# Performance work log

Measured on AMD Instinct MI355X. Metric: run time of the kernel, lower is better.

The kernel has to match this reference:

```python
import jax, jax.numpy as jnp
import numpy as np

ROUTINGS = 3

def squash(s, axis=-1):
    # drives long vectors toward length 1, short vectors toward 0
    norm = jnp.linalg.norm(s, axis=axis, keepdims=True)
    scale = norm ** 2 / (1.0 + norm ** 2) / (norm + 1e-8)
    return scale * s

def dense_capsule(x, W, routings=ROUTINGS):
    # x: [B, I, Di], W: [O, I, Do, Di] -> out: [B, O, Do]
    # torch.matmul(W, x[:,None,:,:,None]).squeeze(-1) == einsum over Di
    x_hat = jnp.einsum('oidc,bic->boid', W, x)          # [B, O, I, Do]
    x_hat_det = jax.lax.stop_gradient(x_hat)
    B, O, I, _ = x_hat.shape
    b = jnp.zeros((B, O, I), dtype=x_hat.dtype)
    outputs = None
    for i in range(routings):
        c = jax.nn.softmax(b, axis=1)                    # [B, O, I]
        if i == routings - 1:
            outputs = squash(jnp.sum(c[..., None] * x_hat, axis=2, keepdims=True))
        else:
            outputs = squash(jnp.sum(c[..., None] * x_hat_det, axis=2, keepdims=True))
            b = b + jnp.sum(outputs * x_hat_det, axis=-1)
    return jnp.squeeze(outputs, axis=2)                  # [B, O, Do]

INIT_NUM_CAP = 128
INIT_DIM_CAP = 8

def setup_inputs() -> dict:
    key = jax.random.key(0)
    k0, k1, k2, k3 = jax.random.split(key, 4)
    x = jax.random.normal(k0, (1024, 1024), dtype=jnp.float32)
    W0 = 0.01 * jax.random.normal(k1, (64, 128, 16, 8), dtype=jnp.float32)
    W1 = 0.01 * jax.random.normal(k2, (32, 64, 32, 16), dtype=jnp.float32)
    W2 = 0.01 * jax.random.normal(k3, (10, 32, 64, 32), dtype=jnp.float32)
    return {"x": x, "W0": W0, "W1": W1, "W2": W2}

def reference(x, W0, W1, W2):
    h = x.reshape(-1, INIT_NUM_CAP, INIT_DIM_CAP)        # [B, 128, 8]
    for W in (W0, W1, W2):
        h = dense_capsule(h, W)
    return jnp.linalg.norm(h, axis=-1)                   # [B, 10]
```

## Files before the change

kernel.cpp:

```cpp
#include <hip/hip_runtime.h>
#include <math.h>

typedef unsigned int u32;

__device__ __forceinline__ u32 pk2(float a, float b){
    u32 ua=__float_as_uint(a), ub=__float_as_uint(b);
    u32 ra=(ua + 0x7fffu + ((ua>>16)&1u))>>16;
    u32 rb=(ub + 0x7fffu + ((ub>>16)&1u))>>16;
    return ra | (rb<<16);
}
__device__ __forceinline__ float lo16(u32 p){ return __uint_as_float(p<<16); }
__device__ __forceinline__ float hi16(u32 p){ return __uint_as_float(p & 0xffff0000u); }

#if __has_builtin(__builtin_amdgcn_fdot2_f32_bf16)
__device__ __forceinline__ float dot2bf(u32 a, u32 b, float c){
    float d;
    asm("v_dot2_f32_bf16 %0, %1, %2, %3" : "=v"(d) : "v"(a), "v"(b), "v"(c));
    return d;
}
#else
__device__ __forceinline__ float dot2bf(u32 a, u32 b, float c){
    return fmaf(hi16(a), hi16(b), fmaf(lo16(a), lo16(b), c));
}
#endif

__device__ __forceinline__ void gll16(const u32* gp, u32* lp){
    __builtin_amdgcn_global_load_lds((const __attribute__((address_space(1))) void*)gp,
                                     (__attribute__((address_space(3))) void*)lp,
                                     16, 0, 0);
}

template<int I,int Di,int O,int Do,int IR>
__global__ void k_conv(const float* __restrict__ W, u32* __restrict__ Wb){
    constexpr int CB=Di/8, LPO=Do/16, GR=LPO*O, NSL=16*CB;
    const int n = O*I*Do*Di/2;
    for (int t = blockIdx.x*blockDim.x+threadIdx.x; t < n; t += gridDim.x*blockDim.x){
        int cw = t & 3;
        int u4 = t >> 2;
        int g    = u4 % GR;  int r1 = u4 / GR;
        int slot = r1 % NSL; int r2 = r1 / NSL;
        int il   = r2 % IR;  int si = r2 / IR;
        int i  = si*IR + il;
        int j  = slot / CB, cb = slot % CB;
        int o  = g % O,     q  = g / O;
        int jg = q*16 + j;
        int c  = cb*8 + cw*2;
        const float* src = W + ((size_t)(o*I + i)*Do + jg)*Di + c;
        Wb[t] = pk2(src[0], src[1]);
    }
}

__global__ void k_pack(const float* __restrict__ x, u32* __restrict__ hb){
    int t = blockIdx.x*blockDim.x + threadIdx.x;
    if (t < 1024*512){
        float2 f = ((const float2*)x)[t];
        hb[t] = pk2(f.x, f.y);
    }
}

template<int I,int Di,int O,int Do,int IR,bool LOGIT>
__global__ __launch_bounds__(512,2) void k_contract(
    const u32* __restrict__ Wb, const u32* __restrict__ hsrc,
    const u32* __restrict__ vsb, u32* __restrict__ ps)
{
    constexpr int CB=Di/8, LPO=Do/16, ACT=O*LPO, GR=LPO*O, NSL=16*CB;
    constexpr int SLICE  = IR*NSL*GR*4;
    constexpr int ROUNDS = SLICE/2048;
    static_assert(SLICE <= 16384, "64KB slab");
    static_assert(SLICE % 2048 == 0, "staging granularity");
    __shared__ __align__(16) u32 slab[SLICE];

    const int tid = threadIdx.x;
    const int w = tid>>6, l = tid&63;
    const int eg = blockIdx.x, sp = blockIdx.y;

    const bool act = l < ACT;
    const int qL = act ? (l%LPO) : 0;
    const int oL = act ? (l/LPO) : 0;
    const int lnoff = qL*O + oL;
    const uint4* W4 = (const uint4*)slab;

    const int e0 = eg*16 + w*2;

    u32 vp[2][8];
    if constexpr (LOGIT){
        #pragma unroll
        for (int k=0;k<2;++k){
            uint4 a = *(const uint4*)(vsb + (size_t)(e0+k)*512 + l*8);
            uint4 b = *(const uint4*)(vsb + (size_t)(e0+k)*512 + l*8 + 4);
            vp[k][0]=a.x; vp[k][1]=a.y; vp[k][2]=a.z; vp[k][3]=a.w;
            vp[k][4]=b.x; vp[k][5]=b.y; vp[k][6]=b.z; vp[k][7]=b.w;
        }
    }

    float sacc[2][16];
    #pragma unroll
    for (int k=0;k<2;++k)
        #pragma unroll
        for (int j=0;j<16;++j) sacc[k][j]=0.f;

    for (int sub=0; sub<2; ++sub){
        if (sub) __syncthreads();
        {
            const u32* g = Wb + (size_t)(sp*2+sub)*SLICE + tid*4;
            u32* ld = slab + w*256;
            #pragma unroll
            for (int rd=0; rd<ROUNDS; ++rd) gll16(g + rd*2048, ld + rd*2048);
        }
        __syncthreads();

        #pragma unroll
        for (int il=0; il<IR; ++il){
            const int i = (sp*2+sub)*IR + il;

            float xh[2][16];
            #pragma unroll
            for (int k=0;k<2;++k)
                #pragma unroll
                for (int j=0;j<16;++j) xh[k][j]=0.f;

            #pragma unroll
            for (int cb=0; cb<CB; ++cb){
                u32 hk[2][4];
                #pragma unroll
                for (int k=0;k<2;++k){
                    uint4 hv = *(const uint4*)(hsrc + (size_t)(e0+k)*512 + i*(Di/2) + cb*4);
                    hk[k][0]=hv.x; hk[k][1]=hv.y; hk[k][2]=hv.z; hk[k][3]=hv.w;
                }
                #pragma unroll
                for (int j=0;j<16;++j){
                    uint4 wv = W4[(il*NSL + j*CB + cb)*GR + lnoff];
                    #pragma unroll
                    for (int k=0;k<2;++k){
                        float t = xh[k][j];
                        t = dot2bf(wv.x, hk[k][0], t);
                        t = dot2bf(wv.y, hk[k][1], t);
                        t = dot2bf(wv.z, hk[k][2], t);
                        t = dot2bf(wv.w, hk[k][3], t);
                        xh[k][j] = t;
                    }
                }
            }

            float cc[2];
            if constexpr (!LOGIT){
                cc[0]=1.f; cc[1]=1.f;
            } else {
                #pragma unroll
                for (int k=0;k<2;++k){
                    float lp=0.f;
                    #pragma unroll
                    for (int jj=0;jj<8;++jj)
                        lp += lo16(vp[k][jj])*xh[k][2*jj] + hi16(vp[k][jj])*xh[k][2*jj+1];
                    if constexpr (LPO>=2) lp += __shfl_xor(lp,1,64);
                    if constexpr (LPO>=4) lp += __shfl_xor(lp,2,64);
                    float ev = act ? __expf(lp) : 0.f;
                    float tot = ev;
                    tot+=__shfl_xor(tot,1,64);  tot+=__shfl_xor(tot,2,64);
                    tot+=__shfl_xor(tot,4,64);  tot+=__shfl_xor(tot,8,64);
                    tot+=__shfl_xor(tot,16,64); tot+=__shfl_xor(tot,32,64);
                    cc[k] = ev*(float)LPO/tot;
                }
            }
            #pragma unroll
            for (int k=0;k<2;++k)
                #pragma unroll
                for (int j=0;j<16;++j) sacc[k][j] += cc[k]*xh[k][j];
        }
    }

    if (act){
        #pragma unroll
        for (int k=0;k<2;++k){
            u32* pp = ps + ((size_t)(sp*1024 + e0 + k))*512 + l*8;
            uint4 o0, o1;
            o0.x=pk2(sacc[k][0],sacc[k][1]);   o0.y=pk2(sacc[k][2],sacc[k][3]);
            o0.z=pk2(sacc[k][4],sacc[k][5]);   o0.w=pk2(sacc[k][6],sacc[k][7]);
            o1.x=pk2(sacc[k][8],sacc[k][9]);   o1.y=pk2(sacc[k][10],sacc[k][11]);
            o1.z=pk2(sacc[k][12],sacc[k][13]); o1.w=pk2(sacc[k][14],sacc[k][15]);
            *(uint4*)pp = o0;
            *(uint4*)(pp+4) = o1;
        }
    }
}

template<int O,int Do,int MODE>
__global__ __launch_bounds__(256) void k_squash(
    const u32* __restrict__ ps, u32* __restrict__ vsb, void* __restrict__ dst)
{
    constexpr int LPO=Do/16, ACT=O*LPO;
    const int tid=threadIdx.x, w=tid>>6, l=tid&63;
    const int e = blockIdx.x*4 + w;
    const bool act = l < ACT;
    const int oL = act ? (l/LPO) : 0;

    float s[16];
    #pragma unroll
    for (int j=0;j<16;++j) s[j]=0.f;
    #pragma unroll
    for (int si=0; si<16; ++si){
        const u32* pp = ps + ((size_t)(si*1024 + e))*512 + l*8;
        uint4 a = *(const uint4*)pp;
        uint4 b = *(const uint4*)(pp+4);
        u32 q[8] = {a.x,a.y,a.z,a.w,b.x,b.y,b.z,b.w};
        #pragma unroll
        for (int k=0;k<8;++k){ s[2*k] += lo16(q[k]); s[2*k+1] += hi16(q[k]); }
    }
    if constexpr (MODE==0){
        #pragma unroll
        for (int j=0;j<16;++j) s[j] *= (1.0f/(float)O);
    }
    float n2=0.f;
    #pragma unroll
    for (int j=0;j<16;++j) n2 += s[j]*s[j];
    if constexpr (LPO>=2) n2 += __shfl_xor(n2,1,64);
    if constexpr (LPO>=4) n2 += __shfl_xor(n2,2,64);
    float nrm   = sqrtf(n2);
    float scale = n2/((1.f+n2)*(nrm+1e-8f));

    if constexpr (MODE==0){
        if (act){
            u32* vp = vsb + (size_t)e*512 + l*8;
            #pragma unroll
            for (int k=0;k<8;++k) vp[k] = pk2(scale*s[2*k], scale*s[2*k+1]);
        }
    } else if constexpr (MODE==1){
        if (act){
            u32* vp = vsb + (size_t)e*512 + l*8;
            #pragma unroll
            for (int k=0;k<8;++k){
                u32 old = vp[k];
                vp[k] = pk2(lo16(old)+scale*s[2*k], hi16(old)+scale*s[2*k+1]);
            }
        }
    } else if constexpr (MODE==2){
        if (act){
            u32* hp = (u32*)dst + (size_t)e*512 + l*8;
            #pragma unroll
            for (int k=0;k<8;++k) hp[k] = pk2(scale*s[2*k], scale*s[2*k+1]);
        }
    } else {
        float q=0.f;
        #pragma unroll
        for (int j=0;j<16;++j){ float vj=scale*s[j]; q += vj*vj; }
        if constexpr (LPO>=2) q += __shfl_xor(q,1,64);
        if constexpr (LPO>=4) q += __shfl_xor(q,2,64);
        if (act && (l%LPO)==0)
            ((float*)dst)[(size_t)e*O + oL] = sqrtf(q);
    }
}

template<int I, int Di, int O, int Do, bool FINAL>
__device__ __forceinline__ void fb_layer(const float* __restrict__ W, float* __restrict__ hl,
                                         float* __restrict__ out, int e, int l) {
    constexpr int LPO = Do / 16;
    constexpr int ACT = O * LPO;
    const int o  = l / LPO;
    const int d0 = (l % LPO) * 16;
    const bool act = (l < ACT);
    float vs[16];
    #pragma unroll
    for (int j = 0; j < 16; ++j) vs[j] = 0.f;
    for (int r = 0; r < 3; ++r) {
        float sacc[16];
        #pragma unroll
        for (int j = 0; j < 16; ++j) sacc[j] = 0.f;
        for (int i = 0; i < I; ++i) {
            if ((i & 15) == 0) __syncthreads();
            float xh[16];
            #pragma unroll
            for (int j = 0; j < 16; ++j) xh[j] = 0.f;
            if (act) {
                const float* wb = W + ((size_t)(o * I + i) * Do + d0) * Di;
                #pragma unroll
                for (int j = 0; j < 16; ++j) {
                    const float4* wr = (const float4*)(wb + j * Di);
                    float acc = 0.f;
                    #pragma unroll
                    for (int c4 = 0; c4 < Di / 4; ++c4) {
                        float4 wv = wr[c4];
                        float4 hv = *(const float4*)(hl + i * Di + c4 * 4);
                        acc += wv.x*hv.x + wv.y*hv.y + wv.z*hv.z + wv.w*hv.w;
                    }
                    xh[j] = acc;
                }
            }
            float cc;
            if (r == 0) cc = 1.0f;
            else {
                float lp = 0.f;
                #pragma unroll
                for (int j = 0; j < 16; ++j) lp += vs[j] * xh[j];
                if constexpr (LPO >= 2) lp += __shfl_xor(lp, 1, 64);
                if constexpr (LPO >= 4) lp += __shfl_xor(lp, 2, 64);
                float ev = act ? __expf(lp) : 0.f;
                float tot = ev;
                tot += __shfl_xor(tot,1,64); tot += __shfl_xor(tot,2,64);
                tot += __shfl_xor(tot,4,64); tot += __shfl_xor(tot,8,64);
                tot += __shfl_xor(tot,16,64); tot += __shfl_xor(tot,32,64);
                cc = ev * (float)LPO / tot;
            }
            #pragma unroll
            for (int j = 0; j < 16; ++j) sacc[j] += cc * xh[j];
        }
        if (r == 0) {
            #pragma unroll
            for (int j = 0; j < 16; ++j) sacc[j] *= (1.0f / O);
        }
        float n2 = 0.f;
        #pragma unroll
        for (int j = 0; j < 16; ++j) n2 += sacc[j] * sacc[j];
        if constexpr (LPO >= 2) n2 += __shfl_xor(n2, 1, 64);
        if constexpr (LPO >= 4) n2 += __shfl_xor(n2, 2, 64);
        float nrm = sqrtf(n2);
        float scale = n2 / ((1.f + n2) * (nrm + 1e-8f));
        if (r < 2) {
            #pragma unroll
            for (int j = 0; j < 16; ++j) vs[j] += scale * sacc[j];
        } else {
            if constexpr (FINAL) {
                float q = 0.f;
                #pragma unroll
                for (int j = 0; j < 16; ++j) { float vj = scale*sacc[j]; q += vj*vj; }
                if constexpr (LPO >= 2) q += __shfl_xor(q, 1, 64);
                if constexpr (LPO >= 4) q += __shfl_xor(q, 2, 64);
                if (act && (l % LPO) == 0) out[(size_t)e * O + o] = sqrtf(q);
            } else {
                __syncthreads();
                if (act) {
                    #pragma unroll
                    for (int j = 0; j < 16; ++j) hl[o * Do + d0 + j] = scale * sacc[j];
                }
                __syncthreads();
            }
        }
    }
}

__global__ __launch_bounds__(256) void fb_caps(const float* __restrict__ x,
                                               const float* __restrict__ W0,
                                               const float* __restrict__ W1,
                                               const float* __restrict__ W2,
                                               float* __restrict__ out) {
    __shared__ float hsh[4][1024];
    const int w = threadIdx.x >> 6;
    const int l = threadIdx.x & 63;
    const int e = blockIdx.x * 4 + w;
    float* hl = hsh[w];
    const float4* xr = (const float4*)(x + (size_t)e * 1024);
    float4* h4 = (float4*)hl;
    #pragma unroll
    for (int k = 0; k < 4; ++k) h4[l + 64 * k] = xr[l + 64 * k];
    __syncthreads();
    fb_layer<128, 8, 64, 16, false>(W0, hl, out, e, l);
    fb_layer<64, 16, 32, 32, false>(W1, hl, out, e, l);
    fb_layer<32, 32, 10, 64, true >(W2, hl, out, e, l);
}

extern "C" void kernel_launch(void* const* d_in, const int* in_sizes, int n_in,
                              void* d_out, int out_size, void* d_ws, size_t ws_size,
                              hipStream_t stream) {
    const float* x  = (const float*)d_in[0];
    const float* W0 = (const float*)d_in[1];
    const float* W1 = (const float*)d_in[2];
    const float* W2 = (const float*)d_in[3];
    float* out = (float*)d_out;

    const size_t DW0 = 524288, DW1 = 524288, DW2 = 327680;
    const size_t DPS = (size_t)16*1024*512;
    const size_t DVS = (size_t)1024*512;
    const size_t DH  = (size_t)1024*512;
    const size_t need = (DW0+DW1+DW2+DPS+DVS+DH)*4;

    if (ws_size < need) {
        fb_caps<<<256, 256, 0, stream>>>(x, W0, W1, W2, out);
        return;
    }

    u32* Wb0 = (u32*)d_ws;
    u32* Wb1 = Wb0 + DW0;
    u32* Wb2 = Wb1 + DW1;
    u32* ps  = Wb2 + DW2;
    u32* vs  = ps  + DPS;
    u32* hb  = vs  + DVS;

    k_conv<128, 8,64,16,4><<<256,256,0,stream>>>(W0, Wb0);
    k_conv< 64,16,32,32,2><<<256,256,0,stream>>>(W1, Wb1);
    k_conv< 32,32,10,64,1><<<256,256,0,stream>>>(W2, Wb2);
    k_pack<<<1024,512,0,stream>>>(x, hb);

    dim3 g(64,16);

    k_contract<128,8,64,16,4,false><<<g,512,0,stream>>>(Wb0, hb, vs, ps);
    k_squash<64,16,0><<<256,256,0,stream>>>(ps, vs, nullptr);
    k_contract<128,8,64,16,4,true ><<<g,512,0,stream>>>(Wb0, hb, vs, ps);
    k_squash<64,16,1><<<256,256,0,stream>>>(ps, vs, nullptr);
    k_contract<128,8,64,16,4,true ><<<g,512,0,stream>>>(Wb0, hb, vs, ps);
    k_squash<64,16,2><<<256,256,0,stream>>>(ps, vs, hb);

    k_contract<64,16,32,32,2,false><<<g,512,0,stream>>>(Wb1, hb, vs, ps);
    k_squash<32,32,0><<<256,256,0,stream>>>(ps, vs, nullptr);
    k_contract<64,16,32,32,2,true ><<<g,512,0,stream>>>(Wb1, hb, vs, ps);
    k_squash<32,32,1><<<256,256,0,stream>>>(ps, vs, nullptr);
    k_contract<64,16,32,32,2,true ><<<g,512,0,stream>>>(Wb1, hb, vs, ps);
    k_squash<32,32,2><<<256,256,0,stream>>>(ps, vs, hb);

    k_contract<32,32,10,64,1,false><<<g,512,0,stream>>>(Wb2, hb, vs, ps);
    k_squash<10,64,0><<<256,256,0,stream>>>(ps, vs, nullptr);
    k_contract<32,32,10,64,1,true ><<<g,512,0,stream>>>(Wb2, hb, vs, ps);
    k_squash<10,64,1><<<256,256,0,stream>>>(ps, vs, nullptr);
    k_contract<32,32,10,64,1,true ><<<g,512,0,stream>>>(Wb2, hb, vs, ps);
    k_squash<10,64,3><<<256,256,0,stream>>>(ps, vs, out);
}
```

Before: 474.1 us.

## Double-buffer weight slabs in LDS and stage the input tile into shared memory

The contraction kernel now splits each block's weight slice into smaller halves and double-buffers them in LDS, prefetching the next half with async global-to-LDS loads while computing on the current one. It also stages the block's whole 16-row input tile into LDS once instead of re-reading it from global memory in the inner loop. LDS use grows to two slabs plus a 32KB input buffer, so launch bounds drop from 2 to 1 block per CU. This trades occupancy for overlapping loads with compute. The weight-layout conversion is simplified to match the new per-i ordering.

```diff
diff --git a/kernel.cpp b/kernel.cpp
--- a/kernel.cpp
+++ b/kernel.cpp
@@ -30,7 +30,7 @@
                                      16, 0, 0);
 }
 
-template<int I,int Di,int O,int Do,int IR>
+template<int I,int Di,int O,int Do>
 __global__ void k_conv(const float* __restrict__ W, u32* __restrict__ Wb){
     constexpr int CB=Di/8, LPO=Do/16, GR=LPO*O, NSL=16*CB;
     const int n = O*I*Do*Di/2;
@@ -38,9 +38,7 @@
         int cw = t & 3;
         int u4 = t >> 2;
         int g    = u4 % GR;  int r1 = u4 / GR;
-        int slot = r1 % NSL; int r2 = r1 / NSL;
-        int il   = r2 % IR;  int si = r2 / IR;
-        int i  = si*IR + il;
+        int slot = r1 % NSL; int i  = r1 / NSL;
         int j  = slot / CB, cb = slot % CB;
         int o  = g % O,     q  = g / O;
         int jg = q*16 + j;
@@ -58,17 +56,19 @@
     }
 }
 
-template<int I,int Di,int O,int Do,int IR,bool LOGIT>
-__global__ __launch_bounds__(512,2) void k_contract(
+template<int I,int Di,int O,int Do,int IRS,int NSUB,bool LOGIT>
+__global__ __launch_bounds__(512,1) void k_contract(
     const u32* __restrict__ Wb, const u32* __restrict__ hsrc,
     const u32* __restrict__ vsb, u32* __restrict__ ps)
 {
     constexpr int CB=Di/8, LPO=Do/16, ACT=O*LPO, GR=LPO*O, NSL=16*CB;
-    constexpr int SLICE  = IR*NSL*GR*4;
-    constexpr int ROUNDS = SLICE/2048;
-    static_assert(SLICE <= 16384, "64KB slab");
-    static_assert(SLICE % 2048 == 0, "staging granularity");
-    __shared__ __align__(16) u32 slab[SLICE];
+    constexpr int HALF   = IRS*NSL*GR*4;
+    constexpr int WRND   = HALF/2048;
+    constexpr int IPB    = IRS*NSUB;
+    static_assert(HALF % 2048 == 0, "staging granularity");
+    static_assert(IPB*16 == I, "i coverage");
+    __shared__ __align__(16) u32 slab[2*HALF];
+    __shared__ __align__(16) u32 hl[8192];
 
     const int tid = threadIdx.x;
     const int w = tid>>6, l = tid&63;
@@ -78,9 +78,24 @@
     const int qL = act ? (l%LPO) : 0;
     const int oL = act ? (l/LPO) : 0;
     const int lnoff = qL*O + oL;
-    const uint4* W4 = (const uint4*)slab;
+
+    auto stage_w = [&](int sub, int buf){
+        const u32* g = Wb + (size_t)(sp*IPB + sub*IRS)*(NSL*GR*4) + tid*4;
+        u32* ld = slab + buf*HALF + w*256;
+        #pragma unroll
+        for (int rd=0; rd<WRND; ++rd) gll16(g + rd*2048, ld + rd*2048);
+    };
+
+    {
+        const u32* g = hsrc + (size_t)eg*8192 + tid*4;
+        u32* ld = hl + w*256;
+        #pragma unroll
+        for (int rd=0; rd<4; ++rd) gll16(g + rd*2048, ld + rd*2048);
+        stage_w(0, 0);
+    }
 
     const int e0 = eg*16 + w*2;
+    const int eL = w*2;
 
     u32 vp[2][8];
     if constexpr (LOGIT){
@@ -99,19 +114,15 @@
         #pragma unroll
         for (int j=0;j<16;++j) sacc[k][j]=0.f;
 
-    for (int sub=0; sub<2; ++sub){
-        if (sub) __syncthreads();
-        {
-            const u32* g = Wb + (size_t)(sp*2+sub)*SLICE + tid*4;
-            u32* ld = slab + w*256;
-            #pragma unroll
-            for (int rd=0; rd<ROUNDS; ++rd) gll16(g + rd*2048, ld + rd*2048);
-        }
-        __syncthreads();
-
-        #pragma unroll
-        for (int il=0; il<IR; ++il){
-            const int i = (sp*2+sub)*IR + il;
+    __syncthreads();
+
+    for (int sub=0; sub<NSUB; ++sub){
+        if (sub+1 < NSUB) stage_w(sub+1, (sub+1)&1);
+        const uint4* W4 = (const uint4*)(slab + (sub&1)*HALF);
+
+        #pragma unroll
+        for (int il=0; il<IRS; ++il){
+            const int i = sp*IPB + sub*IRS + il;
 
             float xh[2][16];
             #pragma unroll
@@ -124,7 +135,7 @@
                 u32 hk[2][4];
                 #pragma unroll
                 for (int k=0;k<2;++k){
-                    uint4 hv = *(const uint4*)(hsrc + (size_t)(e0+k)*512 + i*(Di/2) + cb*4);
+                    uint4 hv = *(const uint4*)&hl[(eL+k)*512 + i*(Di/2) + cb*4];
                     hk[k][0]=hv.x; hk[k][1]=hv.y; hk[k][2]=hv.z; hk[k][3]=hv.w;
                 }
                 #pragma unroll
@@ -167,6 +178,7 @@
                 #pragma unroll
                 for (int j=0;j<16;++j) sacc[k][j] += cc[k]*xh[k][j];
         }
+        __syncthreads();
     }
 
     if (act){
@@ -384,31 +396,31 @@
     u32* vs  = ps  + DPS;
     u32* hb  = vs  + DVS;
 
-    k_conv<128, 8,64,16,4><<<256,256,0,stream>>>(W0, Wb0);
-    k_conv< 64,16,32,32,2><<<256,256,0,stream>>>(W1, Wb1);
-    k_conv< 32,32,10,64,1><<<256,256,0,stream>>>(W2, Wb2);
+    k_conv<128, 8,64,16><<<256,256,0,stream>>>(W0, Wb0);
+    k_conv< 64,16,32,32><<<256,256,0,stream>>>(W1, Wb1);
+    k_conv< 32,32,10,64><<<256,256,0,stream>>>(W2, Wb2);
     k_pack<<<1024,512,0,stream>>>(x, hb);
 
     dim3 g(64,16);
 
-    k_contract<128,8,64,16,4,false><<<g,512,0,stream>>>(Wb0, hb, vs, ps);
+    k_contract<128,8,64,16,2,4,false><<<g,512,0,stream>>>(Wb0, hb, vs, ps);
     k_squash<64,16,0><<<256,256,0,stream>>>(ps, vs, nullptr);
-    k_contract<128,8,64,16,4,true ><<<g,512,0,stream>>>(Wb0, hb, vs, ps);
+    k_contract<128,8,64,16,2,4,true ><<<g,512,0,stream>>>(Wb0, hb, vs, ps);
     k_squash<64,16,1><<<256,256,0,stream>>>(ps, vs, nullptr);
-    k_contract<128,8,64,16,4,true ><<<g,512,0,stream>>>(Wb0, hb, vs, ps);
+    k_contract<128,8,64,16,2,4,true ><<<g,512,0,stream>>>(Wb0, hb, vs, ps);
     k_squash<64,16,2><<<256,256,0,stream>>>(ps, vs, hb);
 
-    k_contract<64,16,32,32,2,false><<<g,512,0,stream>>>(Wb1, hb, vs, ps);
+    k_contract<64,16,32,32,1,4,false><<<g,512,0,stream>>>(Wb1, hb, vs, ps);
     k_squash<32,32,0><<<256,256,0,stream>>>(ps, vs, nullptr);
-    k_contract<64,16,32,32,2,true ><<<g,512,0,stream>>>(Wb1, hb, vs, ps);
+    k_contract<64,16,32,32,1,4,true ><<<g,512,0,stream>>>(Wb1, hb, vs, ps);
     k_squash<32,32,1><<<256,256,0,stream>>>(ps, vs, nullptr);
-    k_contract<64,16,32,32,2,true ><<<g,512,0,stream>>>(Wb1, hb, vs, ps);
+    k_contract<64,16,32,32,1,4,true ><<<g,512,0,stream>>>(Wb1, hb, vs, ps);
     k_squash<32,32,2><<<256,256,0,stream>>>(ps, vs, hb);
 
-    k_contract<32,32,10,64,1,false><<<g,512,0,stream>>>(Wb2, hb, vs, ps);
+    k_contract<32,32,10,64,1,2,false><<<g,512,0,stream>>>(Wb2, hb, vs, ps);
     k_squash<10,64,0><<<256,256,0,stream>>>(ps, vs, nullptr);
-    k_contract<32,32,10,64,1,true ><<<g,512,0,stream>>>(Wb2, hb, vs, ps);
+    k_contract<32,32,10,64,1,2,true ><<<g,512,0,stream>>>(Wb2, hb, vs, ps);
     k_squash<10,64,1><<<256,256,0,stream>>>(ps, vs, nullptr);
-    k_contract<32,32,10,64,1,true ><<<g,512,0,stream>>>(Wb2, hb, vs, ps);
+    k_contract<32,32,10,64,1,2,true ><<<g,512,0,stream>>>(Wb2, hb, vs, ps);
     k_squash<10,64,3><<<256,256,0,stream>>>(ps, vs, out);
 }
```

Measured after the change: 497.0 us. 4.8% more time.

## Fuse routing squash into contract prologue, halve I-splits, merge setup kernels

Applied to the files above, without the earlier changes.

The intermediate squash/update kernels are removed. Each contract kernel now reduces the previous iteration's partial sums and computes the squashed vector in its prologue, and the logit accumulator is kept in vsb, written by the sp==0 blocks. The I dimension is split 8 ways instead of 16, with each block covering four weight slices, so partial-sum traffic is halved and double-buffered psA/psB buffers are used. The weight conversion and x packing kernels are merged into one launch. The cost is that all 8 split blocks redundantly recompute the same squash per element, and each block does more serial work.

```diff
diff --git a/kernel.cpp b/kernel.cpp
--- a/kernel.cpp
+++ b/kernel.cpp
@@ -31,16 +31,17 @@
 }
 
 template<int I,int Di,int O,int Do,int IR>
-__global__ void k_conv(const float* __restrict__ W, u32* __restrict__ Wb){
+__device__ void conv_dev(const float* __restrict__ W, u32* __restrict__ Wb,
+                         int gtid, int gstride){
     constexpr int CB=Di/8, LPO=Do/16, GR=LPO*O, NSL=16*CB;
     const int n = O*I*Do*Di/2;
-    for (int t = blockIdx.x*blockDim.x+threadIdx.x; t < n; t += gridDim.x*blockDim.x){
+    for (int t = gtid; t < n; t += gstride){
         int cw = t & 3;
         int u4 = t >> 2;
         int g    = u4 % GR;  int r1 = u4 / GR;
         int slot = r1 % NSL; int r2 = r1 / NSL;
-        int il   = r2 % IR;  int si = r2 / IR;
-        int i  = si*IR + il;
+        int il   = r2 % IR;  int ss = r2 / IR;
+        int i  = ss*IR + il;
         int j  = slot / CB, cb = slot % CB;
         int o  = g % O,     q  = g / O;
         int jg = q*16 + j;
@@ -50,24 +51,34 @@
     }
 }
 
-__global__ void k_pack(const float* __restrict__ x, u32* __restrict__ hb){
-    int t = blockIdx.x*blockDim.x + threadIdx.x;
-    if (t < 1024*512){
+__global__ void k_setup(const float* __restrict__ W0, const float* __restrict__ W1,
+                        const float* __restrict__ W2, const float* __restrict__ x,
+                        u32* __restrict__ Wb0, u32* __restrict__ Wb1,
+                        u32* __restrict__ Wb2, u32* __restrict__ hb){
+    const int gtid = blockIdx.x*blockDim.x + threadIdx.x;
+    const int gs   = gridDim.x*blockDim.x;
+    conv_dev<128, 8,64,16,4>(W0, Wb0, gtid, gs);
+    conv_dev< 64,16,32,32,2>(W1, Wb1, gtid, gs);
+    conv_dev< 32,32,10,64,1>(W2, Wb2, gtid, gs);
+    for (int t = gtid; t < 1024*512; t += gs){
         float2 f = ((const float2*)x)[t];
         hb[t] = pk2(f.x, f.y);
     }
 }
 
-template<int I,int Di,int O,int Do,int IR,bool LOGIT>
+template<int I,int Di,int O,int Do,int IR,int PRO>
 __global__ __launch_bounds__(512,2) void k_contract(
     const u32* __restrict__ Wb, const u32* __restrict__ hsrc,
-    const u32* __restrict__ vsb, u32* __restrict__ ps)
+    u32* __restrict__ vsb, const u32* __restrict__ ps_in,
+    u32* __restrict__ ps_out)
 {
     constexpr int CB=Di/8, LPO=Do/16, ACT=O*LPO, GR=LPO*O, NSL=16*CB;
-    constexpr int SLICE  = IR*NSL*GR*4;
-    constexpr int ROUNDS = SLICE/2048;
+    constexpr int SUBS  = 4;
+    constexpr int SLICE = IR*NSL*GR*4;
+    constexpr int WRND  = SLICE/2048;
     static_assert(SLICE <= 16384, "64KB slab");
     static_assert(SLICE % 2048 == 0, "staging granularity");
+    static_assert(8*SUBS*IR == I, "i coverage");
     __shared__ __align__(16) u32 slab[SLICE];
 
     const int tid = threadIdx.x;
@@ -78,18 +89,69 @@
     const int qL = act ? (l%LPO) : 0;
     const int oL = act ? (l/LPO) : 0;
     const int lnoff = qL*O + oL;
-    const uint4* W4 = (const uint4*)slab;
+
+    auto stage_w = [&](int sub){
+        const u32* g = Wb + (size_t)(sp*SUBS+sub)*SLICE + tid*4;
+        u32* ld = slab + w*256;
+        #pragma unroll
+        for (int rd=0; rd<WRND; ++rd) gll16(g + rd*2048, ld + rd*2048);
+    };
 
     const int e0 = eg*16 + w*2;
 
+    stage_w(0);
+
     u32 vp[2][8];
-    if constexpr (LOGIT){
+    if constexpr (PRO > 0){
         #pragma unroll
         for (int k=0;k<2;++k){
-            uint4 a = *(const uint4*)(vsb + (size_t)(e0+k)*512 + l*8);
-            uint4 b = *(const uint4*)(vsb + (size_t)(e0+k)*512 + l*8 + 4);
-            vp[k][0]=a.x; vp[k][1]=a.y; vp[k][2]=a.z; vp[k][3]=a.w;
-            vp[k][4]=b.x; vp[k][5]=b.y; vp[k][6]=b.z; vp[k][7]=b.w;
+            const int e = e0+k;
+            float s[16];
+            #pragma unroll
+            for (int j=0;j<16;++j) s[j]=0.f;
+            #pragma unroll
+            for (int si=0; si<8; ++si){
+                const u32* pp = ps_in + ((size_t)(si*1024 + e))*512 + l*8;
+                uint4 a = *(const uint4*)pp;
+                uint4 b = *(const uint4*)(pp+4);
+                u32 q[8]={a.x,a.y,a.z,a.w,b.x,b.y,b.z,b.w};
+                #pragma unroll
+                for (int t2=0;t2<8;++t2){ s[2*t2]+=lo16(q[t2]); s[2*t2+1]+=hi16(q[t2]); }
+            }
+            if constexpr (PRO==1){
+                #pragma unroll
+                for (int j=0;j<16;++j) s[j] *= (1.0f/(float)O);
+            }
+            float n2=0.f;
+            #pragma unroll
+            for (int j=0;j<16;++j) n2 += s[j]*s[j];
+            if constexpr (LPO>=2) n2 += __shfl_xor(n2,1,64);
+            if constexpr (LPO>=4) n2 += __shfl_xor(n2,2,64);
+            float nrm   = sqrtf(n2);
+            float scale = n2/((1.f+n2)*(nrm+1e-8f));
+            float vsv[16];
+            if constexpr (PRO==2){
+                const u32* vr = vsb + (size_t)e*512 + l*8;
+                uint4 a=*(const uint4*)vr; uint4 b=*(const uint4*)(vr+4);
+                u32 q[8]={a.x,a.y,a.z,a.w,b.x,b.y,b.z,b.w};
+                #pragma unroll
+                for (int t2=0;t2<8;++t2){
+                    vsv[2*t2]   = lo16(q[t2]) + scale*s[2*t2];
+                    vsv[2*t2+1] = hi16(q[t2]) + scale*s[2*t2+1];
+                }
+            } else {
+                #pragma unroll
+                for (int j=0;j<16;++j) vsv[j] = scale*s[j];
+            }
+            #pragma unroll
+            for (int jj=0;jj<8;++jj) vp[k][jj] = pk2(vsv[2*jj], vsv[2*jj+1]);
+            if constexpr (PRO==1){
+                if (sp==0 && act){
+                    u32* vw = vsb + (size_t)e*512 + l*8;
+                    #pragma unroll
+                    for (int jj=0;jj<8;++jj) vw[jj] = vp[k][jj];
+                }
+            }
         }
     }
 
@@ -99,19 +161,14 @@
         #pragma unroll
         for (int j=0;j<16;++j) sacc[k][j]=0.f;
 
-    for (int sub=0; sub<2; ++sub){
-        if (sub) __syncthreads();
-        {
-            const u32* g = Wb + (size_t)(sp*2+sub)*SLICE + tid*4;
-            u32* ld = slab + w*256;
-            #pragma unroll
-            for (int rd=0; rd<ROUNDS; ++rd) gll16(g + rd*2048, ld + rd*2048);
-        }
+    for (int sub=0; sub<SUBS; ++sub){
+        if (sub){ __syncthreads(); stage_w(sub); }
         __syncthreads();
+        const uint4* W4 = (const uint4*)slab;
 
         #pragma unroll
         for (int il=0; il<IR; ++il){
-            const int i = (sp*2+sub)*IR + il;
+            const int i = (sp*SUBS+sub)*IR + il;
 
             float xh[2][16];
             #pragma unroll
@@ -143,7 +200,7 @@
             }
 
             float cc[2];
-            if constexpr (!LOGIT){
+            if constexpr (PRO==0){
                 cc[0]=1.f; cc[1]=1.f;
             } else {
                 #pragma unroll
@@ -172,7 +229,7 @@
     if (act){
         #pragma unroll
         for (int k=0;k<2;++k){
-            u32* pp = ps + ((size_t)(sp*1024 + e0 + k))*512 + l*8;
+            u32* pp = ps_out + ((size_t)(sp*1024 + e0 + k))*512 + l*8;
             uint4 o0, o1;
             o0.x=pk2(sacc[k][0],sacc[k][1]);   o0.y=pk2(sacc[k][2],sacc[k][3]);
             o0.z=pk2(sacc[k][4],sacc[k][5]);   o0.w=pk2(sacc[k][6],sacc[k][7]);
@@ -186,7 +243,7 @@
 
 template<int O,int Do,int MODE>
 __global__ __launch_bounds__(256) void k_squash(
-    const u32* __restrict__ ps, u32* __restrict__ vsb, void* __restrict__ dst)
+    const u32* __restrict__ ps, void* __restrict__ dst)
 {
     constexpr int LPO=Do/16, ACT=O*LPO;
     const int tid=threadIdx.x, w=tid>>6, l=tid&63;
@@ -198,17 +255,13 @@
     #pragma unroll
     for (int j=0;j<16;++j) s[j]=0.f;
     #pragma unroll
-    for (int si=0; si<16; ++si){
+    for (int si=0; si<8; ++si){
         const u32* pp = ps + ((size_t)(si*1024 + e))*512 + l*8;
         uint4 a = *(const uint4*)pp;
         uint4 b = *(const uint4*)(pp+4);
         u32 q[8] = {a.x,a.y,a.z,a.w,b.x,b.y,b.z,b.w};
         #pragma unroll
         for (int k=0;k<8;++k){ s[2*k] += lo16(q[k]); s[2*k+1] += hi16(q[k]); }
-    }
-    if constexpr (MODE==0){
-        #pragma unroll
-        for (int j=0;j<16;++j) s[j] *= (1.0f/(float)O);
     }
     float n2=0.f;
     #pragma unroll
@@ -218,22 +271,7 @@
     float nrm   = sqrtf(n2);
     float scale = n2/((1.f+n2)*(nrm+1e-8f));
 
-    if constexpr (MODE==0){
-        if (act){
-            u32* vp = vsb + (size_t)e*512 + l*8;
-            #pragma unroll
-            for (int k=0;k<8;++k) vp[k] = pk2(scale*s[2*k], scale*s[2*k+1]);
-        }
-    } else if constexpr (MODE==1){
-        if (act){
-            u32* vp = vsb + (size_t)e*512 + l*8;
-            #pragma unroll
-            for (int k=0;k<8;++k){
-                u32 old = vp[k];
-                vp[k] = pk2(lo16(old)+scale*s[2*k], hi16(old)+scale*s[2*k+1]);
-            }
-        }
-    } else if constexpr (MODE==2){
+    if constexpr (MODE==2){
         if (act){
             u32* hp = (u32*)dst + (size_t)e*512 + l*8;
             #pragma unroll
@@ -367,10 +405,10 @@
     float* out = (float*)d_out;
 
     const size_t DW0 = 524288, DW1 = 524288, DW2 = 327680;
-    const size_t DPS = (size_t)16*1024*512;
+    const size_t DPS = (size_t)8*1024*512;
     const size_t DVS = (size_t)1024*512;
     const size_t DH  = (size_t)1024*512;
-    const size_t need = (DW0+DW1+DW2+DPS+DVS+DH)*4;
+    const size_t need = (DW0+DW1+DW2 + 2*DPS + DVS + DH)*4;
 
     if (ws_size < need) {
         fb_caps<<<256, 256, 0, stream>>>(x, W0, W1, W2, out);
@@ -380,35 +418,27 @@
     u32* Wb0 = (u32*)d_ws;
     u32* Wb1 = Wb0 + DW0;
     u32* Wb2 = Wb1 + DW1;
-    u32* ps  = Wb2 + DW2;
-    u32* vs  = ps  + DPS;
+    u32* psA = Wb2 + DW2;
+    u32* psB = psA + DPS;
+    u32* vs  = psB + DPS;
     u32* hb  = vs  + DVS;
 
-    k_conv<128, 8,64,16,4><<<256,256,0,stream>>>(W0, Wb0);
-    k_conv< 64,16,32,32,2><<<256,256,0,stream>>>(W1, Wb1);
-    k_conv< 32,32,10,64,1><<<256,256,0,stream>>>(W2, Wb2);
-    k_pack<<<1024,512,0,stream>>>(x, hb);
-
-    dim3 g(64,16);
-
-    k_contract<128,8,64,16,4,false><<<g,512,0,stream>>>(Wb0, hb, vs, ps);
-    k_squash<64,16,0><<<256,256,0,stream>>>(ps, vs, nullptr);
-    k_contract<128,8,64,16,4,true ><<<g,512,0,stream>>>(Wb0, hb, vs, ps);
-    k_squash<64,16,1><<<256,256,0,stream>>>(ps, vs, nullptr);
-    k_contract<128,8,64,16,4,true ><<<g,512,0,stream>>>(Wb0, hb, vs, ps);
-    k_squash<64,16,2><<<256,256,0,stream>>>(ps, vs, hb);
-
-    k_contract<64,16,32,32,2,false><<<g,512,0,stream>>>(Wb1, hb, vs, ps);
-    k_squash<32,32,0><<<256,256,0,stream>>>(ps, vs, nullptr);
-    k_contract<64,16,32,32,2,true ><<<g,512,0,stream>>>(Wb1, hb, vs, ps);
-    k_squash<32,32,1><<<256,256,0,stream>>>(ps, vs, nullptr);
-    k_contract<64,16,32,32,2,true ><<<g,512,0,stream>>>(Wb1, hb, vs, ps);
-    k_squash<32,32,2><<<256,256,0,stream>>>(ps, vs, hb);
-
-    k_contract<32,32,10,64,1,false><<<g,512,0,stream>>>(Wb2, hb, vs, ps);
-    k_squash<10,64,0><<<256,256,0,stream>>>(ps, vs, nullptr);
-    k_contract<32,32,10,64,1,true ><<<g,512,0,stream>>>(Wb2, hb, vs, ps);
-    k_squash<10,64,1><<<256,256,0,stream>>>(ps, vs, nullptr);
-    k_contract<32,32,10,64,1,true ><<<g,512,0,stream>>>(Wb2, hb, vs, ps);
-    k_squash<10,64,3><<<256,256,0,stream>>>(ps, vs, out);
-}
+    k_setup<<<1024, 256, 0, stream>>>(W0, W1, W2, x, Wb0, Wb1, Wb2, hb);
+
+    dim3 g(64, 8);
+
+    k_contract<128,8,64,16,4,0><<<g,512,0,stream>>>(Wb0, hb, vs, nullptr, psA);
+    k_contract<128,8,64,16,4,1><<<g,512,0,stream>>>(Wb0, hb, vs, psA, psB);
+    k_contract<128,8,64,16,4,2><<<g,512,0,stream>>>(Wb0, hb, vs, psB, psA);
+    k_squash<64,16,2><<<256,256,0,stream>>>(psA, hb);
+
+    k_contract<64,16,32,32,2,0><<<g,512,0,stream>>>(Wb1, hb, vs, nullptr, psA);
+    k_contract<64,16,32,32,2,1><<<g,512,0,stream>>>(Wb1, hb, vs, psA, psB);
+    k_contract<64,16,32,32,2,2><<<g,512,0,stream>>>(Wb1, hb, vs, psB, psA);
+    k_squash<32,32,2><<<256,256,0,stream>>>(psA, hb);
+
+    k_contract<32,32,10,64,1,0><<<g,512,0,stream>>>(Wb2, hb, vs, nullptr, psA);
+    k_contract<32,32,10,64,1,1><<<g,512,0,stream>>>(Wb2, hb, vs, psA, psB);
+    k_contract<32,32,10,64,1,2><<<g,512,0,stream>>>(Wb2, hb, vs, psB, psA);
+    k_squash<10,64,3><<<256,256,0,stream>>>(psA, out);
+}
```

New measurement: 458.5 us. -3.3%, faster.
